# Kernel tuning notes

Measured on AMD Instinct MI355X. Metric: run time of the kernel, lower is better.

Reference implementation:

```python
import jax, jax.numpy as jnp
import numpy as np

EMBED_DIM = 1024
NUM_HEADS = 16
HEAD_DIM = EMBED_DIM // NUM_HEADS
FF_DIM = 4 * EMBED_DIM
LN_EPS = 1e-5


def setup_inputs() -> dict:
    key = jax.random.key(0)
    ks = jax.random.split(key, 17)
    s = 0.02
    d = EMBED_DIM
    return {
        "x": jax.random.normal(ks[0], (2, 2048, d), dtype=jnp.float32),
        "Wq": jax.random.normal(ks[1], (d, d), dtype=jnp.float32) * s,
        "bq": jnp.zeros((d,), dtype=jnp.float32),
        "Wk": jax.random.normal(ks[2], (d, d), dtype=jnp.float32) * s,
        "bk": jnp.zeros((d,), dtype=jnp.float32),
        "Wv": jax.random.normal(ks[3], (d, d), dtype=jnp.float32) * s,
        "bv": jnp.zeros((d,), dtype=jnp.float32),
        "Wo": jax.random.normal(ks[4], (d, d), dtype=jnp.float32) * s,
        "bo": jnp.zeros((d,), dtype=jnp.float32),
        "W1": jax.random.normal(ks[5], (d, FF_DIM), dtype=jnp.float32) * s,
        "b1": jnp.zeros((FF_DIM,), dtype=jnp.float32),
        "W2": jax.random.normal(ks[6], (FF_DIM, d), dtype=jnp.float32) * s,
        "b2": jnp.zeros((d,), dtype=jnp.float32),
        "g1": jnp.ones((d,), dtype=jnp.float32),
        "beta1": jnp.zeros((d,), dtype=jnp.float32),
        "g2": jnp.ones((d,), dtype=jnp.float32),
        "beta2": jnp.zeros((d,), dtype=jnp.float32),
    }


def _layer_norm(x, g, b):
    mu = jnp.mean(x, axis=-1, keepdims=True)
    var = jnp.var(x, axis=-1, keepdims=True)
    return (x - mu) * jax.lax.rsqrt(var + LN_EPS) * g + b


def _mhsa(x, Wq, bq, Wk, bk, Wv, bv, Wo, bo):
    B, S, D = x.shape
    q = (x @ Wq + bq).reshape(B, S, NUM_HEADS, HEAD_DIM)
    k = (x @ Wk + bk).reshape(B, S, NUM_HEADS, HEAD_DIM)
    v = (x @ Wv + bv).reshape(B, S, NUM_HEADS, HEAD_DIM)
    # NOTE: original module applies NO 1/sqrt(head_dim) scaling
    scores = jnp.einsum("bqhd,bkhd->bhqk", q, k)  # [B,H,S,S]
    attn = jax.nn.softmax(scores, axis=-1)
    out = jnp.einsum("bhqk,bkhd->bqhd", attn, v).reshape(B, S, D)
    return out @ Wo + bo


def reference(x, Wq, bq, Wk, bk, Wv, bv, Wo, bo, W1, b1, W2, b2, g1, beta1, g2, beta2):
    x = x + _mhsa(x, Wq, bq, Wk, bk, Wv, bv, Wo, bo)
    x = _layer_norm(x, g1, beta1)
    h = jax.nn.gelu(x @ W1 + b1, approximate=False)
    x = x + (h @ W2 + b2)
    x = _layer_norm(x, g2, beta2)
    return x
```

## Files before the change

kernel.cpp:

```cpp
#include <hip/hip_runtime.h>
#include <math.h>

#define SEQ 2048
#define NBATCH 2
#define NHEAD 16
#define HDIM 64
#define DMODEL 1024
#define DFF 4096

typedef __attribute__((ext_vector_type(8))) __bf16 bf16x8;
typedef __attribute__((ext_vector_type(4))) float f32x4;

__device__ __forceinline__ unsigned short f2bf(float f) {
    unsigned int u = __float_as_uint(f);
    u += 0x7FFFu + ((u >> 16) & 1u);
    return (unsigned short)(u >> 16);
}

__device__ __forceinline__ void async16(const unsigned short* g, unsigned short* l) {
    __builtin_amdgcn_global_load_lds(
        (const __attribute__((address_space(1))) unsigned int*)(g),
        (__attribute__((address_space(3))) unsigned int*)(l),
        16, 0, 0);
}

__device__ __forceinline__ void transpose_tile(
    const float* __restrict__ in, unsigned short* __restrict__ out,
    int K, int N, int k0, int n0, int t, unsigned short* sT)
{
    {
        const int r = t >> 4, c4 = t & 15;
#pragma unroll
        for (int i = 0; i < 4; i++) {
            const int k = r + (i << 4);
            const float4 v = *(const float4*)(in + (size_t)(k0 + k) * N + n0 + (c4 << 2));
            sT[((c4 << 2) + 0) * 72 + k] = f2bf(v.x);
            sT[((c4 << 2) + 1) * 72 + k] = f2bf(v.y);
            sT[((c4 << 2) + 2) * 72 + k] = f2bf(v.z);
            sT[((c4 << 2) + 3) * 72 + k] = f2bf(v.w);
        }
    }
    __syncthreads();
    {
        const int n = t >> 2, cc = t & 3;
#pragma unroll
        for (int i = 0; i < 2; i++) {
            const int c = cc + (i << 2);
            *(uint4*)(out + (size_t)(n0 + n) * K + k0 + (c << 3)) =
                *(const uint4*)(&sT[n * 72 + (c << 3)]);
        }
    }
}

__global__ __launch_bounds__(256) void prep_kernel(
    const float* __restrict__ x,
    const float* __restrict__ Wq, const float* __restrict__ Wk,
    const float* __restrict__ Wv, const float* __restrict__ Wo,
    const float* __restrict__ W1, const float* __restrict__ W2,
    const float* __restrict__ bq, const float* __restrict__ bk,
    const float* __restrict__ bv,
    unsigned short* __restrict__ xb, unsigned short* __restrict__ WqkvT,
    unsigned short* __restrict__ WoT, unsigned short* __restrict__ W1T,
    unsigned short* __restrict__ W2T, float* __restrict__ bqkv)
{
    __shared__ unsigned short sT[64 * 72];
    const int bid = blockIdx.x, t = threadIdx.x;
    if (bid < 1024) {
        const int wsel = bid >> 8, tt = bid & 255;
        const float* in = (wsel == 0) ? Wq : (wsel == 1) ? Wk : (wsel == 2) ? Wv : Wo;
        unsigned short* outp = (wsel == 3) ? WoT : WqkvT + (size_t)wsel * 1024 * 1024;
        transpose_tile(in, outp, 1024, 1024, (tt >> 4) << 6, (tt & 15) << 6, t, sT);
    } else if (bid < 2048) {
        const int tt = bid - 1024;
        transpose_tile(W1, W1T, 1024, 4096, (tt >> 6) << 6, (tt & 63) << 6, t, sT);
    } else if (bid < 3072) {
        const int tt = bid - 2048;
        transpose_tile(W2, W2T, 4096, 1024, (tt >> 4) << 6, (tt & 15) << 6, t, sT);
    } else if (bid < 7168) {
        const size_t i = ((size_t)(bid - 3072) * 256 + t) << 2;
        const float4 v = *(const float4*)(x + i);
        ushort4 b;
        b.x = f2bf(v.x); b.y = f2bf(v.y); b.z = f2bf(v.z); b.w = f2bf(v.w);
        *(ushort4*)(xb + i) = b;
    } else {
        const int i = (bid - 7168) * 256 + t;
        float v;
        if (i < 1024)       v = bq[i];
        else if (i < 2048)  v = bk[i - 1024];
        else                v = bv[i - 2048];
        bqkv[i] = v;
    }
}

template<int EPI>
__global__ __launch_bounds__(256) void gemm_bf16_kernel(
    const unsigned short* __restrict__ A, const unsigned short* __restrict__ Bt,
    const float* __restrict__ bias, float* __restrict__ outF,
    unsigned short* __restrict__ outB, unsigned short* __restrict__ outQ,
    unsigned short* __restrict__ outK, unsigned short* __restrict__ outV,
    int N, int K, size_t pstride)
{
    __shared__ unsigned short sA[128 * 64];
    __shared__ unsigned short sB[128 * 64];
    const int gx = gridDim.x, gy = gridDim.y;
    const int flat = blockIdx.y * gx + blockIdx.x;
    const int xcd = flat & 7, slot = flat >> 3;
    const int rx = gx >> 1, ry = gy >> 2;
    const int bx = (xcd & 1) * rx + (slot % rx);
    const int by = (xcd >> 1) * ry + (slot / rx);
    const int m0 = by << 7;
    const int n0 = bx << 7;
    const int kspan = K / gridDim.z;
    const int kbeg = blockIdx.z * kspan;

    const int t = threadIdx.x;
    const int w = t >> 6, l = t & 63, li = l & 15, quad = l >> 4;
    const int wm = (w >> 1) << 6, wn = (w & 1) << 6;
    const int srow = l >> 3;
    const int scol = ((l & 7) ^ srow) << 3;

    f32x4 acc[4][4];
#pragma unroll
    for (int mi = 0; mi < 4; mi++)
#pragma unroll
        for (int ni = 0; ni < 4; ni++)
            acc[mi][ni] = (f32x4){0.f, 0.f, 0.f, 0.f};

    for (int k0 = kbeg; k0 < kbeg + kspan; k0 += 64) {
#pragma unroll
        for (int i = 0; i < 4; i++) {
            const int c = (w << 2) + i;
            async16(A  + (size_t)(m0 + (c << 3) + srow) * K + k0 + scol, &sA[c << 9]);
            async16(Bt + (size_t)(n0 + (c << 3) + srow) * K + k0 + scol, &sB[c << 9]);
        }
        __syncthreads();
#pragma unroll
        for (int ks = 0; ks < 2; ks++) {
            bf16x8 af[4], bfr[4];
#pragma unroll
            for (int mi = 0; mi < 4; mi++)
                af[mi] = *(const bf16x8*)(&sA[((wm + (mi << 4) + li) << 6) +
                                             ((((ks << 2) + quad) ^ (li & 7)) << 3)]);
#pragma unroll
            for (int ni = 0; ni < 4; ni++)
                bfr[ni] = *(const bf16x8*)(&sB[((wn + (ni << 4) + li) << 6) +
                                              ((((ks << 2) + quad) ^ (li & 7)) << 3)]);
#pragma unroll
            for (int mi = 0; mi < 4; mi++)
#pragma unroll
                for (int ni = 0; ni < 4; ni++)
                    acc[mi][ni] = __builtin_amdgcn_mfma_f32_16x16x32_bf16(
                        af[mi], bfr[ni], acc[mi][ni], 0, 0, 0);
        }
        __syncthreads();
    }

    float* outFz = outF + (size_t)blockIdx.z * pstride;
#pragma unroll
    for (int mi = 0; mi < 4; mi++) {
#pragma unroll
        for (int ni = 0; ni < 4; ni++) {
#pragma unroll
            for (int r = 0; r < 4; r++) {
                const int row = m0 + wm + (mi << 4) + (quad << 2) + r;
                const int col = n0 + wn + (ni << 4) + li;
                float v = acc[mi][ni][r];
                if (EPI != 3) v += bias[col];
                if (EPI == 0) {
                    const int b = row >> 11, s = row & 2047;
                    if (col < DMODEL) {
                        const int h = col >> 6, d = col & 63;
                        outQ[(((size_t)(b * NHEAD + h) * SEQ + s) << 6) + d] = f2bf(v);
                    } else if (col < 2 * DMODEL) {
                        const int c = col - DMODEL, h = c >> 6, d = c & 63;
                        outK[(((size_t)(b * NHEAD + h) * SEQ + s) << 6) + d] = f2bf(v);
                    } else {
                        const int c = col - 2 * DMODEL, h = c >> 6, d = c & 63;
                        outV[(((size_t)(b * NHEAD + h) * HDIM + d) << 11) + s] = f2bf(v);
                    }
                } else if (EPI == 2) {
                    outB[(size_t)row * N + col] =
                        f2bf(0.5f * v * (1.0f + erff(v * 0.70710678118654752f)));
                } else {
                    outFz[(size_t)row * N + col] = v;
                }
            }
        }
    }
}

__global__ __launch_bounds__(256) void attn_kernel(
    const unsigned short* __restrict__ Qb, const unsigned short* __restrict__ Kb,
    const unsigned short* __restrict__ Vt, unsigned short* __restrict__ AOb)
{
    __shared__ unsigned short sK[2][64 * 64];
    __shared__ unsigned short sV[2][64 * 64];
    __shared__ unsigned short sP[4][32 * 72];
    const int t = threadIdx.x, w = t >> 6, l = t & 63;
    const int li = l & 15, quad = l >> 4;
    const int p = blockIdx.x;
    const int xcd = p & 7, slot = p >> 3;
    const int bh = (xcd << 2) + (slot >> 4);
    const int q0 = (slot & 15) << 7;
    const unsigned short* Qh = Qb + ((size_t)bh << 17);
    const unsigned short* Kh = Kb + ((size_t)bh << 17);
    const unsigned short* Vh = Vt + ((size_t)bh << 17);
    const int qw = q0 + (w << 5);
    const int ssw = ((l & 7) ^ (l >> 3)) << 3;

    bf16x8 aq[2][2];
#pragma unroll
    for (int m = 0; m < 2; m++)
#pragma unroll
        for (int h = 0; h < 2; h++)
            aq[m][h] = *(const bf16x8*)(Qh + ((size_t)(qw + (m << 4) + li) << 6) + (h << 5) + (quad << 3));

    bf16x8 bone;
#pragma unroll
    for (int j = 0; j < 8; j++) bone[j] = (__bf16)1.0f;

    f32x4 o[2][4];
    f32x4 accl[2];
#pragma unroll
    for (int m = 0; m < 2; m++) {
        accl[m] = (f32x4){0.f, 0.f, 0.f, 0.f};
#pragma unroll
        for (int d = 0; d < 4; d++) o[m][d] = (f32x4){0.f, 0.f, 0.f, 0.f};
    }
    const f32x4 z = (f32x4){0.f, 0.f, 0.f, 0.f};
    unsigned short* myP = &sP[w][0];

#define STAGE(buf, kc)                                                              \
    {                                                                               \
        _Pragma("unroll")                                                           \
        for (int i = 0; i < 4; i++) {                                               \
            const int cc = (w << 2) + i;                                            \
            if (cc < 8)                                                             \
                async16(Kh + ((size_t)((kc) + (cc << 3) + (l >> 3)) << 6) + ssw,    \
                        &sK[buf][cc << 9]);                                         \
            else                                                                    \
                async16(Vh + ((size_t)(((cc - 8) << 3) + (l >> 3)) << 11) + (kc) + ssw, \
                        &sV[buf][(cc - 8) << 9]);                                   \
        }                                                                           \
    }

    STAGE(0, 0);
    __syncthreads();

    for (int kc = 0, it = 0; kc < SEQ; kc += 64, it++) {
        const int cur = it & 1;
        if (kc + 64 < SEQ) STAGE(cur ^ 1, kc + 64);

        f32x4 sc[2][4];
#pragma unroll
        for (int nt = 0; nt < 4; nt++) {
            const bf16x8 bk0 = *(const bf16x8*)(&sK[cur][(((nt << 4) + li) << 6) +
                                                         ((quad ^ (li & 7)) << 3)]);
            const bf16x8 bk1 = *(const bf16x8*)(&sK[cur][(((nt << 4) + li) << 6) +
                                                         (((4 + quad) ^ (li & 7)) << 3)]);
#pragma unroll
            for (int m = 0; m < 2; m++) {
                sc[m][nt] = __builtin_amdgcn_mfma_f32_16x16x32_bf16(aq[m][0], bk0, z, 0, 0, 0);
                sc[m][nt] = __builtin_amdgcn_mfma_f32_16x16x32_bf16(aq[m][1], bk1, sc[m][nt], 0, 0, 0);
            }
        }
#pragma unroll
        for (int m = 0; m < 2; m++)
#pragma unroll
            for (int nt = 0; nt < 4; nt++)
#pragma unroll
                for (int r = 0; r < 4; r++)
                    myP[((m << 4) + (quad << 2) + r) * 72 + (nt << 4) + li] =
                        f2bf(__expf(sc[m][nt][r]));

        bf16x8 ap[2][2];
#pragma unroll
        for (int m = 0; m < 2; m++)
#pragma unroll
            for (int h = 0; h < 2; h++)
                ap[m][h] = *(const bf16x8*)(myP + ((m << 4) + li) * 72 + (h << 5) + (quad << 3));

#pragma unroll
        for (int m = 0; m < 2; m++) {
            accl[m] = __builtin_amdgcn_mfma_f32_16x16x32_bf16(ap[m][0], bone, accl[m], 0, 0, 0);
            accl[m] = __builtin_amdgcn_mfma_f32_16x16x32_bf16(ap[m][1], bone, accl[m], 0, 0, 0);
        }
#pragma unroll
        for (int dt = 0; dt < 4; dt++) {
#pragma unroll
            for (int h = 0; h < 2; h++) {
                const bf16x8 bv = *(const bf16x8*)(&sV[cur][(((dt << 4) + li) << 6) +
                                                            ((((h << 2) + quad) ^ (li & 7)) << 3)]);
#pragma unroll
                for (int m = 0; m < 2; m++)
                    o[m][dt] = __builtin_amdgcn_mfma_f32_16x16x32_bf16(ap[m][h], bv, o[m][dt], 0, 0, 0);
            }
        }
        __syncthreads();
    }

    const int b = bh >> 4, h = bh & 15;
#pragma unroll
    for (int m = 0; m < 2; m++)
#pragma unroll
        for (int dt = 0; dt < 4; dt++)
#pragma unroll
            for (int r = 0; r < 4; r++) {
                const int row = qw + (m << 4) + (quad << 2) + r;
                const int col = (h << 6) + (dt << 4) + li;
                AOb[((size_t)b * SEQ + row) * DMODEL + col] = f2bf(o[m][dt][r] / accl[m][r]);
            }
}

__global__ __launch_bounds__(256) void ln_fuse_kernel(
    const float* __restrict__ P0, const float* __restrict__ P1,
    const float* __restrict__ resid, const float* __restrict__ bias,
    const float* __restrict__ g, const float* __restrict__ be,
    float* __restrict__ outF, unsigned short* __restrict__ outB)
{
    __shared__ float red[8];
    const int row = blockIdx.x, t = threadIdx.x;
    const size_t base = (size_t)row * DMODEL + (t << 2);
    const float4 a = *(const float4*)(P0 + base);
    const float4 b = *(const float4*)(P1 + base);
    const float4 c = *(const float4*)(resid + base);
    const float4 bi = *(const float4*)(bias + (t << 2));
    float4 v;
    v.x = a.x + b.x + c.x + bi.x;
    v.y = a.y + b.y + c.y + bi.y;
    v.z = a.z + b.z + c.z + bi.z;
    v.w = a.w + b.w + c.w + bi.w;
    float s = v.x + v.y + v.z + v.w;
    float s2 = v.x * v.x + v.y * v.y + v.z * v.z + v.w * v.w;
#pragma unroll
    for (int m = 1; m < 64; m <<= 1) {
        s += __shfl_xor(s, m, 64);
        s2 += __shfl_xor(s2, m, 64);
    }
    if ((t & 63) == 0) { red[t >> 6] = s; red[4 + (t >> 6)] = s2; }
    __syncthreads();
    s = red[0] + red[1] + red[2] + red[3];
    s2 = red[4] + red[5] + red[6] + red[7];
    const float mu = s * (1.0f / 1024.0f);
    const float var = s2 * (1.0f / 1024.0f) - mu * mu;
    const float rs = rsqrtf(var + 1e-5f);
    const float4 gg = *(const float4*)(g + (t << 2));
    const float4 bb = *(const float4*)(be + (t << 2));
    float4 ov;
    ov.x = (v.x - mu) * rs * gg.x + bb.x;
    ov.y = (v.y - mu) * rs * gg.y + bb.y;
    ov.z = (v.z - mu) * rs * gg.z + bb.z;
    ov.w = (v.w - mu) * rs * gg.w + bb.w;
    *(float4*)(outF + base) = ov;
    if (outB) {
        ushort4 ob;
        ob.x = f2bf(ov.x); ob.y = f2bf(ov.y); ob.z = f2bf(ov.z); ob.w = f2bf(ov.w);
        *(ushort4*)(outB + base) = ob;
    }
}

extern "C" void kernel_launch(void* const* d_in, const int* in_sizes, int n_in,
                              void* d_out, int out_size, void* d_ws, size_t ws_size,
                              hipStream_t stream)
{
    (void)in_sizes; (void)n_in; (void)out_size; (void)ws_size;
    const float* x   = (const float*)d_in[0];
    const float* Wq  = (const float*)d_in[1];
    const float* bq  = (const float*)d_in[2];
    const float* Wk  = (const float*)d_in[3];
    const float* bk  = (const float*)d_in[4];
    const float* Wv  = (const float*)d_in[5];
    const float* bv  = (const float*)d_in[6];
    const float* Wo  = (const float*)d_in[7];
    const float* bo  = (const float*)d_in[8];
    const float* W1  = (const float*)d_in[9];
    const float* b1  = (const float*)d_in[10];
    const float* W2  = (const float*)d_in[11];
    const float* b2  = (const float*)d_in[12];
    const float* g1  = (const float*)d_in[13];
    const float* be1 = (const float*)d_in[14];
    const float* g2  = (const float*)d_in[15];
    const float* be2 = (const float*)d_in[16];
    float* out = (float*)d_out;

    char* ws = (char*)d_ws;
    unsigned short* WqkvT = (unsigned short*)(ws + 0);
    unsigned short* WoT   = (unsigned short*)(ws + 6291456);
    unsigned short* W1T   = (unsigned short*)(ws + 8388608);
    unsigned short* W2T   = (unsigned short*)(ws + 16777216);
    float* bqkv           = (float*)(ws + 25165824);
    unsigned short* xb    = (unsigned short*)(ws + 25178112);
    unsigned short* Qb    = (unsigned short*)(ws + 33566720);
    unsigned short* Kb    = (unsigned short*)(ws + 41955328);
    unsigned short* Vt    = (unsigned short*)(ws + 50343936);
    unsigned short* AOb   = (unsigned short*)(ws + 58732544);
    float* x1             = (float*)(ws + 67121152);
    unsigned short* x1b   = (unsigned short*)(ws + 83898368);
    unsigned short* hb    = (unsigned short*)(ws + 92286976);
    float* Po0 = (float*)(ws + 92286976);
    float* Po1 = (float*)(ws + 92286976 + 16777216);
    float* Pf0 = (float*)(ws + 33566720);
    float* Pf1 = (float*)(ws + 50343936);

    prep_kernel<<<7180, 256, 0, stream>>>(
        x, Wq, Wk, Wv, Wo, W1, W2, bq, bk, bv,
        xb, WqkvT, WoT, W1T, W2T, bqkv);

    gemm_bf16_kernel<0><<<dim3(24, 32), 256, 0, stream>>>(
        xb, WqkvT, bqkv, nullptr, nullptr, Qb, Kb, Vt, 3072, 1024, 0);

    attn_kernel<<<512, 256, 0, stream>>>(Qb, Kb, Vt, AOb);

    gemm_bf16_kernel<3><<<dim3(8, 32, 2), 256, 0, stream>>>(
        AOb, WoT, nullptr, Po0, nullptr, nullptr, nullptr, nullptr, 1024, 1024,
        (size_t)4096 * 1024);

    ln_fuse_kernel<<<4096, 256, 0, stream>>>(Po0, Po1, x, bo, g1, be1, x1, x1b);

    gemm_bf16_kernel<2><<<dim3(32, 32), 256, 0, stream>>>(
        x1b, W1T, b1, nullptr, hb, nullptr, nullptr, nullptr, 4096, 1024, 0);

    gemm_bf16_kernel<3><<<dim3(8, 32, 2), 256, 0, stream>>>(
        hb, W2T, nullptr, Pf0, nullptr, nullptr, nullptr, nullptr, 1024, 4096,
        (size_t)4096 * 1024);

    ln_fuse_kernel<<<4096, 256, 0, stream>>>(Pf0, Pf1, x1, b2, g2, be2, out, nullptr);
}
```

Before: 382.6 us.

## Halve attention query tile per block, vectorize V-transpose stores, use tanh GELU

The attention kernel now gives each wave 16 query rows instead of 32, with 64 queries per block, and launches twice as many blocks. The P scratch buffer uses an XOR-swizzled 64-wide layout in place of padding. The QKV GEMM epilogue is specialised so that V-transposed outputs are written as packed 4-element stores with the bias hoisted per column. The FF1 epilogue replaces erf GELU with a tanh/exp approximation. The aim is better occupancy and cheaper epilogues, at the cost of twice the K/V staging traffic per query and a small numerical deviation from exact GELU.

```diff
diff --git a/kernel.cpp b/kernel.cpp
--- a/kernel.cpp
+++ b/kernel.cpp
@@ -155,34 +155,59 @@
         __syncthreads();
     }
 
-    float* outFz = outF + (size_t)blockIdx.z * pstride;
-#pragma unroll
-    for (int mi = 0; mi < 4; mi++) {
+    if (EPI == 0) {
+        const int region = n0 >> 10;
+        const int bq_ = m0 >> 11;
+        const int sloc = (m0 & 2047) + wm + (quad << 2);
 #pragma unroll
         for (int ni = 0; ni < 4; ni++) {
-#pragma unroll
-            for (int r = 0; r < 4; r++) {
-                const int row = m0 + wm + (mi << 4) + (quad << 2) + r;
-                const int col = n0 + wn + (ni << 4) + li;
-                float v = acc[mi][ni][r];
-                if (EPI != 3) v += bias[col];
-                if (EPI == 0) {
-                    const int b = row >> 11, s = row & 2047;
-                    if (col < DMODEL) {
-                        const int h = col >> 6, d = col & 63;
-                        outQ[(((size_t)(b * NHEAD + h) * SEQ + s) << 6) + d] = f2bf(v);
-                    } else if (col < 2 * DMODEL) {
-                        const int c = col - DMODEL, h = c >> 6, d = c & 63;
-                        outK[(((size_t)(b * NHEAD + h) * SEQ + s) << 6) + d] = f2bf(v);
+            const int col = n0 + wn + (ni << 4) + li;
+            const int c = col & 1023;
+            const int h = c >> 6, d = c & 63;
+            const float bcol = bias[col];
+            if (region < 2) {
+                unsigned short* base = ((region == 0) ? outQ : outK) +
+                    (((size_t)(bq_ * NHEAD + h)) << 17) + d;
+#pragma unroll
+                for (int mi = 0; mi < 4; mi++)
+#pragma unroll
+                    for (int r = 0; r < 4; r++)
+                        base[(size_t)(sloc + (mi << 4) + r) << 6] =
+                            f2bf(acc[mi][ni][r] + bcol);
+            } else {
+                unsigned short* base = outV + (((size_t)(bq_ * NHEAD + h)) << 17) +
+                    ((size_t)d << 11) + sloc;
+#pragma unroll
+                for (int mi = 0; mi < 4; mi++) {
+                    ushort4 pk;
+                    pk.x = f2bf(acc[mi][ni][0] + bcol);
+                    pk.y = f2bf(acc[mi][ni][1] + bcol);
+                    pk.z = f2bf(acc[mi][ni][2] + bcol);
+                    pk.w = f2bf(acc[mi][ni][3] + bcol);
+                    *(ushort4*)(base + (mi << 4)) = pk;
+                }
+            }
+        }
+    } else {
+        float* outFz = outF + (size_t)blockIdx.z * pstride;
+#pragma unroll
+        for (int mi = 0; mi < 4; mi++) {
+#pragma unroll
+            for (int ni = 0; ni < 4; ni++) {
+#pragma unroll
+                for (int r = 0; r < 4; r++) {
+                    const int row = m0 + wm + (mi << 4) + (quad << 2) + r;
+                    const int col = n0 + wn + (ni << 4) + li;
+                    float v = acc[mi][ni][r];
+                    if (EPI == 2) {
+                        v += bias[col];
+                        const float tt = 0.79788456080286536f *
+                                         (v + 0.044715f * v * v * v);
+                        const float ge = v / (1.0f + __expf(-2.0f * tt));
+                        outB[(size_t)row * N + col] = f2bf(ge);
                     } else {
-                        const int c = col - 2 * DMODEL, h = c >> 6, d = c & 63;
-                        outV[(((size_t)(b * NHEAD + h) * HDIM + d) << 11) + s] = f2bf(v);
+                        outFz[(size_t)row * N + col] = v;
                     }
-                } else if (EPI == 2) {
-                    outB[(size_t)row * N + col] =
-                        f2bf(0.5f * v * (1.0f + erff(v * 0.70710678118654752f)));
-                } else {
-                    outFz[(size_t)row * N + col] = v;
                 }
             }
         }
@@ -195,38 +220,33 @@
 {
     __shared__ unsigned short sK[2][64 * 64];
     __shared__ unsigned short sV[2][64 * 64];
-    __shared__ unsigned short sP[4][32 * 72];
+    __shared__ unsigned short sP[4][16 * 64];
     const int t = threadIdx.x, w = t >> 6, l = t & 63;
     const int li = l & 15, quad = l >> 4;
     const int p = blockIdx.x;
     const int xcd = p & 7, slot = p >> 3;
-    const int bh = (xcd << 2) + (slot >> 4);
-    const int q0 = (slot & 15) << 7;
+    const int bh = (xcd << 2) + (slot >> 5);
+    const int q0 = (slot & 31) << 6;
     const unsigned short* Qh = Qb + ((size_t)bh << 17);
     const unsigned short* Kh = Kb + ((size_t)bh << 17);
     const unsigned short* Vh = Vt + ((size_t)bh << 17);
-    const int qw = q0 + (w << 5);
+    const int qw = q0 + (w << 4);
     const int ssw = ((l & 7) ^ (l >> 3)) << 3;
-
-    bf16x8 aq[2][2];
-#pragma unroll
-    for (int m = 0; m < 2; m++)
-#pragma unroll
-        for (int h = 0; h < 2; h++)
-            aq[m][h] = *(const bf16x8*)(Qh + ((size_t)(qw + (m << 4) + li) << 6) + (h << 5) + (quad << 3));
+    const int lq7 = li & 7;
+
+    bf16x8 aq[2];
+#pragma unroll
+    for (int h = 0; h < 2; h++)
+        aq[h] = *(const bf16x8*)(Qh + ((size_t)(qw + li) << 6) + (h << 5) + (quad << 3));
 
     bf16x8 bone;
 #pragma unroll
     for (int j = 0; j < 8; j++) bone[j] = (__bf16)1.0f;
 
-    f32x4 o[2][4];
-    f32x4 accl[2];
-#pragma unroll
-    for (int m = 0; m < 2; m++) {
-        accl[m] = (f32x4){0.f, 0.f, 0.f, 0.f};
-#pragma unroll
-        for (int d = 0; d < 4; d++) o[m][d] = (f32x4){0.f, 0.f, 0.f, 0.f};
-    }
+    f32x4 o[4];
+    f32x4 accl = (f32x4){0.f, 0.f, 0.f, 0.f};
+#pragma unroll
+    for (int d = 0; d < 4; d++) o[d] = (f32x4){0.f, 0.f, 0.f, 0.f};
     const f32x4 z = (f32x4){0.f, 0.f, 0.f, 0.f};
     unsigned short* myP = &sP[w][0];
 
@@ -251,49 +271,39 @@
         const int cur = it & 1;
         if (kc + 64 < SEQ) STAGE(cur ^ 1, kc + 64);
 
-        f32x4 sc[2][4];
+        f32x4 sc[4];
 #pragma unroll
         for (int nt = 0; nt < 4; nt++) {
             const bf16x8 bk0 = *(const bf16x8*)(&sK[cur][(((nt << 4) + li) << 6) +
-                                                         ((quad ^ (li & 7)) << 3)]);
+                                                         ((quad ^ lq7) << 3)]);
             const bf16x8 bk1 = *(const bf16x8*)(&sK[cur][(((nt << 4) + li) << 6) +
-                                                         (((4 + quad) ^ (li & 7)) << 3)]);
-#pragma unroll
-            for (int m = 0; m < 2; m++) {
-                sc[m][nt] = __builtin_amdgcn_mfma_f32_16x16x32_bf16(aq[m][0], bk0, z, 0, 0, 0);
-                sc[m][nt] = __builtin_amdgcn_mfma_f32_16x16x32_bf16(aq[m][1], bk1, sc[m][nt], 0, 0, 0);
+                                                         (((4 + quad) ^ lq7) << 3)]);
+            sc[nt] = __builtin_amdgcn_mfma_f32_16x16x32_bf16(aq[0], bk0, z, 0, 0, 0);
+            sc[nt] = __builtin_amdgcn_mfma_f32_16x16x32_bf16(aq[1], bk1, sc[nt], 0, 0, 0);
+        }
+#pragma unroll
+        for (int nt = 0; nt < 4; nt++)
+#pragma unroll
+            for (int r = 0; r < 4; r++) {
+                const int row = (quad << 2) + r;
+                myP[(row << 6) + ((((nt << 1) + (li >> 3)) ^ (row & 7)) << 3) + lq7] =
+                    f2bf(__expf(sc[nt][r]));
             }
-        }
-#pragma unroll
-        for (int m = 0; m < 2; m++)
-#pragma unroll
-            for (int nt = 0; nt < 4; nt++)
-#pragma unroll
-                for (int r = 0; r < 4; r++)
-                    myP[((m << 4) + (quad << 2) + r) * 72 + (nt << 4) + li] =
-                        f2bf(__expf(sc[m][nt][r]));
-
-        bf16x8 ap[2][2];
-#pragma unroll
-        for (int m = 0; m < 2; m++)
-#pragma unroll
-            for (int h = 0; h < 2; h++)
-                ap[m][h] = *(const bf16x8*)(myP + ((m << 4) + li) * 72 + (h << 5) + (quad << 3));
-
-#pragma unroll
-        for (int m = 0; m < 2; m++) {
-            accl[m] = __builtin_amdgcn_mfma_f32_16x16x32_bf16(ap[m][0], bone, accl[m], 0, 0, 0);
-            accl[m] = __builtin_amdgcn_mfma_f32_16x16x32_bf16(ap[m][1], bone, accl[m], 0, 0, 0);
-        }
+
+        bf16x8 ap[2];
+#pragma unroll
+        for (int h = 0; h < 2; h++)
+            ap[h] = *(const bf16x8*)(myP + (li << 6) + ((((h << 2) + quad) ^ lq7) << 3));
+
+        accl = __builtin_amdgcn_mfma_f32_16x16x32_bf16(ap[0], bone, accl, 0, 0, 0);
+        accl = __builtin_amdgcn_mfma_f32_16x16x32_bf16(ap[1], bone, accl, 0, 0, 0);
 #pragma unroll
         for (int dt = 0; dt < 4; dt++) {
 #pragma unroll
             for (int h = 0; h < 2; h++) {
                 const bf16x8 bv = *(const bf16x8*)(&sV[cur][(((dt << 4) + li) << 6) +
-                                                            ((((h << 2) + quad) ^ (li & 7)) << 3)]);
-#pragma unroll
-                for (int m = 0; m < 2; m++)
-                    o[m][dt] = __builtin_amdgcn_mfma_f32_16x16x32_bf16(ap[m][h], bv, o[m][dt], 0, 0, 0);
+                                                            ((((h << 2) + quad) ^ lq7) << 3)]);
+                o[dt] = __builtin_amdgcn_mfma_f32_16x16x32_bf16(ap[h], bv, o[dt], 0, 0, 0);
             }
         }
         __syncthreads();
@@ -301,15 +311,13 @@
 
     const int b = bh >> 4, h = bh & 15;
 #pragma unroll
-    for (int m = 0; m < 2; m++)
-#pragma unroll
-        for (int dt = 0; dt < 4; dt++)
-#pragma unroll
-            for (int r = 0; r < 4; r++) {
-                const int row = qw + (m << 4) + (quad << 2) + r;
-                const int col = (h << 6) + (dt << 4) + li;
-                AOb[((size_t)b * SEQ + row) * DMODEL + col] = f2bf(o[m][dt][r] / accl[m][r]);
-            }
+    for (int dt = 0; dt < 4; dt++)
+#pragma unroll
+        for (int r = 0; r < 4; r++) {
+            const int row = qw + (quad << 2) + r;
+            const int col = (h << 6) + (dt << 4) + li;
+            AOb[((size_t)b * SEQ + row) * DMODEL + col] = f2bf(o[dt][r] / accl[r]);
+        }
 }
 
 __global__ __launch_bounds__(256) void ln_fuse_kernel(
@@ -409,7 +417,7 @@
     gemm_bf16_kernel<0><<<dim3(24, 32), 256, 0, stream>>>(
         xb, WqkvT, bqkv, nullptr, nullptr, Qb, Kb, Vt, 3072, 1024, 0);
 
-    attn_kernel<<<512, 256, 0, stream>>>(Qb, Kb, Vt, AOb);
+    attn_kernel<<<1024, 256, 0, stream>>>(Qb, Kb, Vt, AOb);
 
     gemm_bf16_kernel<3><<<dim3(8, 32, 2), 256, 0, stream>>>(
         AOb, WoT, nullptr, Po0, nullptr, nullptr, nullptr, nullptr, 1024, 1024,
```

New measurement: 374.8 us. 2.0% less time.
